# Performance work log

Measured on AMD Instinct MI355X. Metric: run time of the kernel, lower is better.

## Reference

```python
import jax, jax.numpy as jnp
import numpy as np

EPS = 1e-5

def conv1d(x, w, b, pad):
    # x: (B,Cin,T), w: (Cout,Cin,K)
    y = jax.lax.conv_general_dilated(x, w, (1,), [(pad, pad)],
                                     dimension_numbers=('NCW', 'OIW', 'NCW'))
    return y + b[None, :, None]

def group_norm(x, scale, bias, groups):
    B, C, T = x.shape
    xg = x.reshape(B, groups, C // groups, T)
    mu = xg.mean(axis=(2, 3), keepdims=True)
    var = xg.var(axis=(2, 3), keepdims=True)
    xn = ((xg - mu) * jax.lax.rsqrt(var + EPS)).reshape(B, C, T)
    return xn * scale[None, :, None] + bias[None, :, None]

def setup_inputs() -> dict:
    key = jax.random.key(0)
    ks = jax.random.split(key, 16)
    T, B = 1024, 128
    class_size, style_size, char_style_size = 80, 256, 64
    hidden, n_out = 128, 1
    cin = class_size + style_size + char_style_size  # 400
    def w(k, shape, fan_in):
        return jax.random.normal(k, shape, jnp.float32) * (1.0 / np.sqrt(fan_in))
    inp = {
        'input': jax.random.normal(ks[0], (T, B, class_size), jnp.float32),
        'g_style': jax.random.normal(ks[1], (B, style_size), jnp.float32),
        'spacing_style': jax.random.normal(ks[2], (B, 8), jnp.float32),
        'char_style': jax.random.normal(ks[3], (B, class_size, char_style_size), jnp.float32),
        'conv1_w': w(ks[4], (hidden, cin, 3), cin * 3),
        'conv1_b': jnp.zeros((hidden,), jnp.float32),
        'gn1_s': jnp.ones((hidden,), jnp.float32),
        'gn1_b': jnp.zeros((hidden,), jnp.float32),
        'conv2_w': w(ks[5], (hidden // 2, hidden, 3), hidden * 3),
        'conv2_b': jnp.zeros((hidden // 2,), jnp.float32),
        'gn2_s': jnp.ones((hidden // 2,), jnp.float32),
        'gn2_b': jnp.zeros((hidden // 2,), jnp.float32),
        'conv3_w': w(ks[6], (hidden // 4, hidden // 2, 3), (hidden // 2) * 3),
        'conv3_b': jnp.zeros((hidden // 4,), jnp.float32),
        'gn3_s': jnp.ones((hidden // 4,), jnp.float32),
        'gn3_b': jnp.zeros((hidden // 4,), jnp.float32),
        'conv4_w': w(ks[7], (n_out, hidden // 4, 1), hidden // 4),
        'conv4_b': jnp.zeros((n_out,), jnp.float32),
        'mean': jnp.full((1, n_out), 2.0, jnp.float32),
        'std': jnp.full((1, n_out), 1.0, jnp.float32),
    }
    return inp

def reference(input, g_style, spacing_style, char_style,
              conv1_w, conv1_b, gn1_s, gn1_b,
              conv2_w, conv2_b, gn2_s, gn2_b,
              conv3_w, conv3_b, gn3_s, gn3_b,
              conv4_w, conv4_b, mean, std):
    T, B, _ = input.shape
    # vectorized char-style gather (replaces the python double loop)
    text_chars = jnp.argmax(input, axis=2)                      # (T,B)
    input_style = char_style[jnp.arange(B)[None, :], text_chars]  # (T,B,Dc)
    gs = jnp.broadcast_to(g_style[None], (T,) + g_style.shape)    # (T,B,Ds)
    x = jnp.concatenate([input, gs, input_style], axis=2)         # (T,B,Cin)
    x = x.transpose(1, 2, 0)                                      # (B,Cin,T)
    x = jax.nn.relu(group_norm(conv1d(x, conv1_w, conv1_b, 1), gn1_s, gn1_b, 32))
    x = jax.nn.relu(group_norm(conv1d(x, conv2_w, conv2_b, 1), gn2_s, gn2_b, 32))
    x = jax.nn.relu(group_norm(conv1d(x, conv3_w, conv3_b, 1), gn3_s, gn3_b, 32))
    x = conv1d(x, conv4_w, conv4_b, 0)                            # (B,n_out,T)
    out = x.transpose(2, 0, 1)                                    # (T,B,n_out)
    return out * std + mean
```

## Files before the change

### kernel.cpp

```cpp
#include <hip/hip_runtime.h>
#include <hip/hip_bf16.h>

#define T_LEN 1024
#define BATCH 128
#define NM 131072

typedef __attribute__((ext_vector_type(8))) short short8;
typedef __attribute__((ext_vector_type(4))) float f32x4;

__device__ __forceinline__ float b2f(ushort u) {
  union { uint i; float f; } c; c.i = ((uint)u) << 16; return c.f;
}
__device__ __forceinline__ ushort f2b(float f) {
  __hip_bfloat16 h = __float2bfloat16(f);
  return *reinterpret_cast<ushort*>(&h);
}
__device__ __forceinline__ uint pack2(float a, float b) {
  return (uint)f2b(a) | ((uint)f2b(b) << 16);
}

__global__ __launch_bounds__(256) void k_prep(const float* __restrict__ inp, const float* __restrict__ cs,
    const float* __restrict__ gsty,
    const float* __restrict__ w1, const float* __restrict__ b1,
    const float* __restrict__ w2, const float* __restrict__ w3,
    ushort* __restrict__ X1, float* __restrict__ Gfull, float* __restrict__ Gk0, float* __restrict__ Gk2,
    ushort* __restrict__ Wp1, ushort* __restrict__ Wp2, ushort* __restrict__ Wp3) {
  int bid = blockIdx.x, tid = threadIdx.x;
  if (bid < 2048) {
    int m = bid * 64 + (tid >> 2);
    int q = tid & 3;
    int t = m >> 7, b = m & 127;
    const float* row = inp + (size_t)m * 80 + q * 20;
    float v[20];
    #pragma unroll
    for (int i = 0; i < 5; ++i) {
      float4 u = *(const float4*)(row + i*4);
      v[i*4+0]=u.x; v[i*4+1]=u.y; v[i*4+2]=u.z; v[i*4+3]=u.w;
    }
    float best = v[0]; int bi = q*20;
    #pragma unroll
    for (int i = 1; i < 20; ++i) if (v[i] > best) { best = v[i]; bi = q*20 + i; }
    #pragma unroll
    for (int d = 1; d <= 2; d <<= 1) {
      float ob = __shfl_xor(best, d);
      int   oi = __shfl_xor(bi, d);
      if (ob > best || (ob == best && oi < bi)) { best = ob; bi = oi; }
    }
    ushort* orow = X1 + ((size_t)b*1024 + t)*160;
    #pragma unroll
    for (int i = 0; i < 5; ++i) {
      uint2 pk; pk.x = pack2(v[i*4], v[i*4+1]); pk.y = pack2(v[i*4+2], v[i*4+3]);
      *(uint2*)(orow + q*20 + i*4) = pk;
    }
    *(uint2*)(orow + 80 + q*4) = make_uint2(0u, 0u);
    const float* crow = cs + ((size_t)b*80 + bi)*64 + q*16;
    #pragma unroll
    for (int i = 0; i < 4; ++i) {
      float4 u = *(const float4*)(crow + i*4);
      uint2 pk; pk.x = pack2(u.x, u.y); pk.y = pack2(u.z, u.w);
      *(uint2*)(orow + 96 + q*16 + i*4) = pk;
    }
  } else if (bid < 2176) {
    int b = bid - 2048;
    __shared__ float gl[256];
    gl[tid] = gsty[b*256 + tid];
    __syncthreads();
    if (tid < 128) {
      int o = tid;
      const float* wr = w1 + (size_t)o*1200 + 240;
      float s0 = 0.f, s1 = 0.f, s2 = 0.f;
      for (int c = 0; c < 256; ++c) {
        float g = gl[c];
        s0 += wr[c*3+0]*g; s1 += wr[c*3+1]*g; s2 += wr[c*3+2]*g;
      }
      Gk0[b*128+o] = s0;
      Gk2[b*128+o] = s2;
      Gfull[b*128+o] = s0 + s1 + s2 + b1[o];
    }
  } else {
    int e = (bid - 2176)*256 + tid;
    if (e < 61440) {
      int o = e / 480, r = e % 480, k = r / 160, c = r % 160;
      float v = 0.f;
      if (c < 80)       v = w1[(size_t)o*1200 + c*3 + k];
      else if (c >= 96) v = w1[(size_t)o*1200 + (336 + (c-96))*3 + k];
      Wp1[e] = f2b(v);
    } else if (e < 61440 + 24576) {
      int e2 = e - 61440;
      int o = e2/384, r = e2%384, k = r/128, c = r%128;
      Wp2[e2] = f2b(w2[(size_t)o*384 + c*3 + k]);
    } else if (e < 61440 + 24576 + 6144) {
      int e3 = e - 61440 - 24576;
      int o = e3/192, r = e3%192, k = r/64, c = r%64;
      Wp3[e3] = f2b(w3[(size_t)o*192 + c*3 + k]);
    }
  }
}

__device__ __forceinline__ uint4 c1_ldx(const ushort* X1b, int cc, int t0, int task) {
  int r = task >> 2, q = task & 3;
  int t = t0 - 1 + r;
  if (t >= 0 && t < T_LEN) return *(const uint4*)(X1b + (size_t)t*160 + cc*32 + q*8);
  return make_uint4(0u,0u,0u,0u);
}
__device__ __forceinline__ short8 c1_ldw(const ushort* Wp1, int cc, int task) {
  int o = task / 12, seg = task % 12;
  int k = seg >> 2, oct = seg & 3;
  return *(const short8*)(Wp1 + (size_t)o*480 + k*160 + cc*32 + oct*8);
}
__device__ __forceinline__ void c1_wrx(ushort (*Xsb)[40], int task, uint4 v) {
  int r = task >> 2, q = task & 3;
  *(uint4*)&Xsb[r][q*8] = v;
}
__device__ __forceinline__ void c1_wrw(ushort (*Wsb)[104], int task, short8 v) {
  int o = task / 12, seg = task % 12;
  *(short8*)&Wsb[o][seg*8] = v;
}

__global__ __launch_bounds__(256) void k_conv1(const ushort* __restrict__ X1, const ushort* __restrict__ Wp1,
    const float* __restrict__ Gfull, const float* __restrict__ Gk0, const float* __restrict__ Gk2,
    ushort* __restrict__ y1, float2* __restrict__ part1) {
  __shared__ __align__(16) ushort Xs[2][130][40];
  __shared__ __align__(16) ushort Ws[2][128][104];
  __shared__ float gf[128], g0v[128], g2v[128];
  __shared__ float ps[4][128], pq[4][128];
  int b = blockIdx.x, tt = blockIdx.y;
  int t0 = tt * 128;
  int tid = threadIdx.x, lane = tid & 63, wave = tid >> 6;
  int ln = lane & 15, lq = lane >> 4, wt = wave * 32;
  const ushort* X1b = X1 + (size_t)b * 163840;

  if (tid < 128) {
    gf[tid]  = Gfull[b*128 + tid];
    g0v[tid] = Gk0[b*128 + tid];
    g2v[tid] = Gk2[b*128 + tid];
  }
  f32x4 acc[2][8];
  #pragma unroll
  for (int m = 0; m < 2; ++m)
    #pragma unroll
    for (int n = 0; n < 8; ++n) { f32x4 z = {0.f,0.f,0.f,0.f}; acc[m][n] = z; }

  uint4 rx0, rx1, rx2;
  short8 rw[6];

  rx0 = c1_ldx(X1b, 0, t0, tid);
  rx1 = c1_ldx(X1b, 0, t0, tid + 256);
  if (tid < 8) rx2 = c1_ldx(X1b, 0, t0, tid + 512);
  #pragma unroll
  for (int i = 0; i < 6; ++i) rw[i] = c1_ldw(Wp1, 0, tid + i*256);
  c1_wrx(Xs[0], tid, rx0);
  c1_wrx(Xs[0], tid + 256, rx1);
  if (tid < 8) c1_wrx(Xs[0], tid + 512, rx2);
  #pragma unroll
  for (int i = 0; i < 6; ++i) c1_wrw(Ws[0], tid + i*256, rw[i]);
  __syncthreads();

  for (int cc = 0; cc < 5; ++cc) {
    bool more = (cc < 4);
    if (more) {
      rx0 = c1_ldx(X1b, cc+1, t0, tid);
      rx1 = c1_ldx(X1b, cc+1, t0, tid + 256);
      if (tid < 8) rx2 = c1_ldx(X1b, cc+1, t0, tid + 512);
      #pragma unroll
      for (int i = 0; i < 6; ++i) rw[i] = c1_ldw(Wp1, cc+1, tid + i*256);
    }
    int cur = cc & 1;
    #pragma unroll
    for (int k = 0; k < 3; ++k) {
      short8 a0 = *(const short8*)&Xs[cur][wt + ln + k][lq*8];
      short8 a1 = *(const short8*)&Xs[cur][wt + 16 + ln + k][lq*8];
      #pragma unroll
      for (int nt = 0; nt < 8; ++nt) {
        short8 bb = *(const short8*)&Ws[cur][nt*16 + ln][k*32 + lq*8];
        acc[0][nt] = __builtin_amdgcn_mfma_f32_16x16x32_bf16(a0, bb, acc[0][nt], 0, 0, 0);
        acc[1][nt] = __builtin_amdgcn_mfma_f32_16x16x32_bf16(a1, bb, acc[1][nt], 0, 0, 0);
      }
    }
    if (more) {
      int nxt = cur ^ 1;
      c1_wrx(Xs[nxt], tid, rx0);
      c1_wrx(Xs[nxt], tid + 256, rx1);
      if (tid < 8) c1_wrx(Xs[nxt], tid + 512, rx2);
      #pragma unroll
      for (int i = 0; i < 6; ++i) c1_wrw(Ws[nxt], tid + i*256, rw[i]);
    }
    __syncthreads();
  }

  #pragma unroll
  for (int nt = 0; nt < 8; ++nt) {
    int o = nt*16 + ln;
    float add = gf[o];
    float s = 0.f, sq = 0.f;
    #pragma unroll
    for (int mt = 0; mt < 2; ++mt) {
      int tb = t0 + wt + mt*16 + lq*4;
      float vv[4];
      #pragma unroll
      for (int r = 0; r < 4; ++r) {
        float v = acc[mt][nt][r] + add;
        int t = tb + r;
        if (t == 0) v -= g0v[o];
        if (t == T_LEN-1) v -= g2v[o];
        vv[r] = v; s += v; sq += v*v;
      }
      uint2 pk;
      pk.x = pack2(vv[0], vv[1]);
      pk.y = pack2(vv[2], vv[3]);
      *(uint2*)(y1 + ((size_t)b*128 + o)*T_LEN + tb) = pk;
    }
    s  += __shfl_xor(s, 16);  s  += __shfl_xor(s, 32);
    sq += __shfl_xor(sq, 16); sq += __shfl_xor(sq, 32);
    if (lane < 16) { ps[wave][o] = s; pq[wave][o] = sq; }
  }
  __syncthreads();
  if (tid < 128) {
    float S = ps[0][tid]+ps[1][tid]+ps[2][tid]+ps[3][tid];
    float Q = pq[0][tid]+pq[1][tid]+pq[2][tid]+pq[3][tid];
    part1[((size_t)b*128 + tid)*8 + tt] = make_float2(S, Q);
  }
}

__device__ __forceinline__ short8 mid_ldw(const ushort* Wp, int cin, int cc, int task) {
  int o = task / 12, seg = task % 12;
  int k = seg >> 2, oct = seg & 3;
  return *(const short8*)(Wp + ((size_t)o*3 + k)*cin + cc*32 + oct*8);
}
__device__ __forceinline__ void mid_wrw(ushort (*Wsb)[104], int task, short8 v) {
  int o = task / 12, seg = task % 12;
  *(short8*)&Wsb[o][seg*8] = v;
}

template<int NC, int CO, int NT, int CPG>
__global__ __launch_bounds__(256) void k_convmid(const ushort* __restrict__ xin,
    const ushort* __restrict__ Wp, const float* __restrict__ bias,
    const float2* __restrict__ partin, const float* __restrict__ gs, const float* __restrict__ gb,
    ushort* __restrict__ yout, float2* __restrict__ part) {
  constexpr int CIN = NC*32;
  constexpr int NG = CIN/CPG;
  __shared__ __align__(16) ushort Xs[2][130][40];
  __shared__ __align__(16) ushort Ws[2][CO][104];
  __shared__ float2 affl[CIN];
  __shared__ float ssb[CIN], qqb[CIN];
  __shared__ float2 gmr[NG];
  __shared__ float bl[CO];
  __shared__ float ps[4][CO], pq[4][CO];
  int b = blockIdx.x, tt = blockIdx.y, t0 = tt*128;
  int tid = threadIdx.x, lane = tid & 63, wave = tid >> 6;
  int ln = lane & 15, lq = lane >> 4, wt = wave*32;
  int cp = (tid & 15)*2, j = tid >> 4;
  int er = (tid < 32) ? 0 : 129, eci = tid & 31;
  const ushort* xb = xin + (size_t)b * CIN * T_LEN;

  if (tid < CIN) {
    const float2* p = partin + (size_t)(b*CIN + tid)*8;
    float S = 0.f, Q = 0.f;
    #pragma unroll
    for (int j2 = 0; j2 < 8; ++j2) { float2 v = p[j2]; S += v.x; Q += v.y; }
    ssb[tid] = S; qqb[tid] = Q;
  }
  if (tid < CO)  bl[tid]  = bias[tid];

  f32x4 acc[2][NT];
  #pragma unroll
  for (int m = 0; m < 2; ++m)
    #pragma unroll
    for (int n = 0; n < NT; ++n) { f32x4 z = {0.f,0.f,0.f,0.f}; acc[m][n] = z; }

  short8 v0, v1;
  ushort ev = 0;
  short8 rw0, rw1, rw2;
  int te = t0 - 1 + er;

  {
    const ushort* s0 = xb + (size_t)cp * T_LEN + t0 + j*8;
    v0 = *(const short8*)s0;
    v1 = *(const short8*)(s0 + T_LEN);
    ev = 0;
    if (tid < 64 && te >= 0 && te < T_LEN) ev = xb[(size_t)eci * T_LEN + te];
    rw0 = mid_ldw(Wp, CIN, 0, tid);
    if constexpr (CO == 64) {
      rw1 = mid_ldw(Wp, CIN, 0, tid + 256);
      rw2 = mid_ldw(Wp, CIN, 0, tid + 512);
    } else {
      if (tid < 128) rw1 = mid_ldw(Wp, CIN, 0, tid + 256);
    }
  }
  __syncthreads();
  if (tid < NG) {
    float S = 0.f, Q = 0.f;
    #pragma unroll
    for (int ci = 0; ci < CPG; ++ci) { S += ssb[tid*CPG+ci]; Q += qqb[tid*CPG+ci]; }
    float invn = 1.f / (float)(CPG * T_LEN);
    float m = S * invn;
    float var = Q * invn - m*m;
    gmr[tid] = make_float2(m, rsqrtf(var + 1e-5f));
  }
  __syncthreads();
  if (tid < CIN) {
    float2 mr = gmr[tid / CPG];
    float a = mr.y * gs[tid];
    affl[tid] = make_float2(a, gb[tid] - mr.x * a);
  }
  __syncthreads();
  {
    float2 A0 = affl[cp], A1 = affl[cp+1];
    #pragma unroll
    for (int e = 0; e < 8; ++e) {
      float f0 = fmaxf(0.f, b2f((ushort)v0[e])*A0.x + A0.y);
      float f1 = fmaxf(0.f, b2f((ushort)v1[e])*A1.x + A1.y);
      *(uint*)&Xs[0][1 + j*8 + e][cp] = pack2(f0, f1);
    }
    if (tid < 64) {
      ushort val = 0;
      if (te >= 0 && te < T_LEN) { float2 A = affl[eci]; val = f2b(fmaxf(0.f, b2f(ev)*A.x + A.y)); }
      Xs[0][er][eci] = val;
    }
    mid_wrw(Ws[0], tid, rw0);
    if constexpr (CO == 64) {
      mid_wrw(Ws[0], tid + 256, rw1);
      mid_wrw(Ws[0], tid + 512, rw2);
    } else {
      if (tid < 128) mid_wrw(Ws[0], tid + 256, rw1);
    }
  }
  __syncthreads();

  for (int cc = 0; cc < NC; ++cc) {
    bool more = (cc + 1 < NC);
    if (more) {
      const ushort* s0 = xb + (size_t)((cc+1)*32 + cp) * T_LEN + t0 + j*8;
      v0 = *(const short8*)s0;
      v1 = *(const short8*)(s0 + T_LEN);
      ev = 0;
      if (tid < 64 && te >= 0 && te < T_LEN) ev = xb[(size_t)((cc+1)*32 + eci) * T_LEN + te];
      rw0 = mid_ldw(Wp, CIN, cc+1, tid);
      if constexpr (CO == 64) {
        rw1 = mid_ldw(Wp, CIN, cc+1, tid + 256);
        rw2 = mid_ldw(Wp, CIN, cc+1, tid + 512);
      } else {
        if (tid < 128) rw1 = mid_ldw(Wp, CIN, cc+1, tid + 256);
      }
    }
    int cur = cc & 1;
    #pragma unroll
    for (int k = 0; k < 3; ++k) {
      short8 a0 = *(const short8*)&Xs[cur][wt + ln + k][lq*8];
      short8 a1 = *(const short8*)&Xs[cur][wt + 16 + ln + k][lq*8];
      #pragma unroll
      for (int nt = 0; nt < NT; ++nt) {
        short8 bb = *(const short8*)&Ws[cur][nt*16 + ln][k*32 + lq*8];
        acc[0][nt] = __builtin_amdgcn_mfma_f32_16x16x32_bf16(a0, bb, acc[0][nt], 0, 0, 0);
        acc[1][nt] = __builtin_amdgcn_mfma_f32_16x16x32_bf16(a1, bb, acc[1][nt], 0, 0, 0);
      }
    }
    if (more) {
      int nxt = cur ^ 1;
      float2 A0 = affl[(cc+1)*32 + cp], A1 = affl[(cc+1)*32 + cp + 1];
      #pragma unroll
      for (int e = 0; e < 8; ++e) {
        float f0 = fmaxf(0.f, b2f((ushort)v0[e])*A0.x + A0.y);
        float f1 = fmaxf(0.f, b2f((ushort)v1[e])*A1.x + A1.y);
        *(uint*)&Xs[nxt][1 + j*8 + e][cp] = pack2(f0, f1);
      }
      if (tid < 64) {
        ushort val = 0;
        if (te >= 0 && te < T_LEN) { float2 A = affl[(cc+1)*32 + eci]; val = f2b(fmaxf(0.f, b2f(ev)*A.x + A.y)); }
        Xs[nxt][er][eci] = val;
      }
      mid_wrw(Ws[nxt], tid, rw0);
      if constexpr (CO == 64) {
        mid_wrw(Ws[nxt], tid + 256, rw1);
        mid_wrw(Ws[nxt], tid + 512, rw2);
      } else {
        if (tid < 128) mid_wrw(Ws[nxt], tid + 256, rw1);
      }
    }
    __syncthreads();
  }

  #pragma unroll
  for (int nt = 0; nt < NT; ++nt) {
    int o = nt*16 + ln;
    float add = bl[o];
    float s = 0.f, sq = 0.f;
    #pragma unroll
    for (int mt = 0; mt < 2; ++mt) {
      int tb = t0 + wt + mt*16 + lq*4;
      float vv[4];
      #pragma unroll
      for (int r = 0; r < 4; ++r) {
        float v = acc[mt][nt][r] + add;
        vv[r] = v; s += v; sq += v*v;
      }
      uint2 pk;
      pk.x = pack2(vv[0], vv[1]);
      pk.y = pack2(vv[2], vv[3]);
      *(uint2*)(yout + ((size_t)b*CO + o)*T_LEN + tb) = pk;
    }
    s  += __shfl_xor(s, 16);  s  += __shfl_xor(s, 32);
    sq += __shfl_xor(sq, 16); sq += __shfl_xor(sq, 32);
    if (lane < 16) { ps[wave][o] = s; pq[wave][o] = sq; }
  }
  __syncthreads();
  if (tid < CO) {
    float S = ps[0][tid]+ps[1][tid]+ps[2][tid]+ps[3][tid];
    float Q = pq[0][tid]+pq[1][tid]+pq[2][tid]+pq[3][tid];
    part[((size_t)b*CO + tid)*8 + tt] = make_float2(S, Q);
  }
}

__global__ __launch_bounds__(256) void k_final(const ushort* __restrict__ y3, const float2* __restrict__ part3,
    const float* __restrict__ s3, const float* __restrict__ b3,
    const float* __restrict__ w4, const float* __restrict__ b4,
    const float* __restrict__ mn, const float* __restrict__ sd, float* __restrict__ out) {
  int b = blockIdx.x;
  int t = blockIdx.y * 256 + threadIdx.x;
  __shared__ float wl[32];
  __shared__ float2 al[32];
  if (threadIdx.x < 32) {
    int c = threadIdx.x;
    const float2* p = part3 + (size_t)(b*32 + c)*8;
    float S = 0.f, Q = 0.f;
    #pragma unroll
    for (int j = 0; j < 8; ++j) { float2 v = p[j]; S += v.x; Q += v.y; }
    float invn = 1.f / (float)T_LEN;
    float m = S * invn;
    float var = Q * invn - m*m;
    float rs = rsqrtf(var + 1e-5f);
    float a = rs * s3[c];
    al[c] = make_float2(a, b3[c] - m*a);
    wl[c] = w4[c];
  }
  __syncthreads();
  float s = b4[0];
  #pragma unroll 8
  for (int c = 0; c < 32; ++c) {
    float v = b2f(y3[((size_t)b*32 + c)*T_LEN + t]);
    float2 A = al[c];
    s += wl[c] * fmaxf(0.f, v*A.x + A.y);
  }
  out[(size_t)t*BATCH + b] = s*sd[0] + mn[0];
}

extern "C" void kernel_launch(void* const* d_in, const int* in_sizes, int n_in,
                              void* d_out, int out_size, void* d_ws, size_t ws_size,
                              hipStream_t stream) {
  const float* inp  = (const float*)d_in[0];
  const float* gsty = (const float*)d_in[1];
  const float* cs   = (const float*)d_in[3];
  const float* w1   = (const float*)d_in[4];
  const float* b1   = (const float*)d_in[5];
  const float* gn1s = (const float*)d_in[6];
  const float* gn1b = (const float*)d_in[7];
  const float* w2   = (const float*)d_in[8];
  const float* b2   = (const float*)d_in[9];
  const float* gn2s = (const float*)d_in[10];
  const float* gn2b = (const float*)d_in[11];
  const float* w3   = (const float*)d_in[12];
  const float* b3   = (const float*)d_in[13];
  const float* gn3s = (const float*)d_in[14];
  const float* gn3b = (const float*)d_in[15];
  const float* w4   = (const float*)d_in[16];
  const float* b4   = (const float*)d_in[17];
  const float* mn   = (const float*)d_in[18];
  const float* sd   = (const float*)d_in[19];
  float* out = (float*)d_out;
  ushort* wsu = (ushort*)d_ws;

  ushort* X1  = wsu;
  ushort* Wp1 = X1 + (size_t)20971520;
  ushort* Wp2 = Wp1 + 61440;
  ushort* Wp3 = Wp2 + 24576;
  float* Gfull = (float*)(Wp3 + 6144);
  float* Gk0   = Gfull + 16384;
  float* Gk2   = Gk0 + 16384;
  ushort* y1 = (ushort*)(Gk2 + 16384);
  ushort* y2 = y1 + (size_t)NM*128;
  ushort* y3 = y2 + (size_t)NM*64;
  float2* part1 = (float2*)(y3 + (size_t)NM*32);
  float2* part2 = part1 + 131072;
  float2* part3 = part2 + 65536;

  k_prep<<<2536, 256, 0, stream>>>(inp, cs, gsty, w1, b1, w2, w3,
                                   X1, Gfull, Gk0, Gk2, Wp1, Wp2, Wp3);
  k_conv1<<<dim3(128,8), 256, 0, stream>>>(X1, Wp1, Gfull, Gk0, Gk2, y1, part1);
  k_convmid<4,64,4,4><<<dim3(128,8), 256, 0, stream>>>(y1, Wp2, b2, part1, gn1s, gn1b, y2, part2);
  k_convmid<2,32,2,2><<<dim3(128,8), 256, 0, stream>>>(y2, Wp3, b3, part2, gn2s, gn2b, y3, part3);
  k_final<<<dim3(128,4), 256, 0, stream>>>(y3, part3, gn3s, gn3b, w4, b4, mn, sd, out);
}
```

Before: 98.53 us.

## Fuse input argmax/gather/concat staging into conv1 shared-memory load

Moves the argmax, char-style gather and bf16 packing of the conv1 input out of the prep kernel and into k_conv1, which now stages all 160 channels for its time tile (plus halo) directly into shared memory. This removes the write and re-read of the ~40MB X1 intermediate in global memory and shrinks the prep grid. In exchange, halo rows are recomputed by neighbouring tiles, the X tile is no longer double-buffered, and each conv1 block does more scattered fp32 loads up front before compute.

```diff
diff --git a/kernel.cpp b/kernel.cpp
--- a/kernel.cpp
+++ b/kernel.cpp
@@ -19,49 +19,14 @@
   return (uint)f2b(a) | ((uint)f2b(b) << 16);
 }
 
-__global__ __launch_bounds__(256) void k_prep(const float* __restrict__ inp, const float* __restrict__ cs,
-    const float* __restrict__ gsty,
+__global__ __launch_bounds__(256) void k_prep(const float* __restrict__ gsty,
     const float* __restrict__ w1, const float* __restrict__ b1,
     const float* __restrict__ w2, const float* __restrict__ w3,
-    ushort* __restrict__ X1, float* __restrict__ Gfull, float* __restrict__ Gk0, float* __restrict__ Gk2,
+    float* __restrict__ Gfull, float* __restrict__ Gk0, float* __restrict__ Gk2,
     ushort* __restrict__ Wp1, ushort* __restrict__ Wp2, ushort* __restrict__ Wp3) {
   int bid = blockIdx.x, tid = threadIdx.x;
-  if (bid < 2048) {
-    int m = bid * 64 + (tid >> 2);
-    int q = tid & 3;
-    int t = m >> 7, b = m & 127;
-    const float* row = inp + (size_t)m * 80 + q * 20;
-    float v[20];
-    #pragma unroll
-    for (int i = 0; i < 5; ++i) {
-      float4 u = *(const float4*)(row + i*4);
-      v[i*4+0]=u.x; v[i*4+1]=u.y; v[i*4+2]=u.z; v[i*4+3]=u.w;
-    }
-    float best = v[0]; int bi = q*20;
-    #pragma unroll
-    for (int i = 1; i < 20; ++i) if (v[i] > best) { best = v[i]; bi = q*20 + i; }
-    #pragma unroll
-    for (int d = 1; d <= 2; d <<= 1) {
-      float ob = __shfl_xor(best, d);
-      int   oi = __shfl_xor(bi, d);
-      if (ob > best || (ob == best && oi < bi)) { best = ob; bi = oi; }
-    }
-    ushort* orow = X1 + ((size_t)b*1024 + t)*160;
-    #pragma unroll
-    for (int i = 0; i < 5; ++i) {
-      uint2 pk; pk.x = pack2(v[i*4], v[i*4+1]); pk.y = pack2(v[i*4+2], v[i*4+3]);
-      *(uint2*)(orow + q*20 + i*4) = pk;
-    }
-    *(uint2*)(orow + 80 + q*4) = make_uint2(0u, 0u);
-    const float* crow = cs + ((size_t)b*80 + bi)*64 + q*16;
-    #pragma unroll
-    for (int i = 0; i < 4; ++i) {
-      float4 u = *(const float4*)(crow + i*4);
-      uint2 pk; pk.x = pack2(u.x, u.y); pk.y = pack2(u.z, u.w);
-      *(uint2*)(orow + 96 + q*16 + i*4) = pk;
-    }
-  } else if (bid < 2176) {
-    int b = bid - 2048;
+  if (bid < 128) {
+    int b = bid;
     __shared__ float gl[256];
     gl[tid] = gsty[b*256 + tid];
     __syncthreads();
@@ -78,7 +43,7 @@
       Gfull[b*128+o] = s0 + s1 + s2 + b1[o];
     }
   } else {
-    int e = (bid - 2176)*256 + tid;
+    int e = (bid - 128)*256 + tid;
     if (e < 61440) {
       int o = e / 480, r = e % 480, k = r / 160, c = r % 160;
       float v = 0.f;
@@ -97,30 +62,62 @@
   }
 }
 
-__device__ __forceinline__ uint4 c1_ldx(const ushort* X1b, int cc, int t0, int task) {
-  int r = task >> 2, q = task & 3;
-  int t = t0 - 1 + r;
-  if (t >= 0 && t < T_LEN) return *(const uint4*)(X1b + (size_t)t*160 + cc*32 + q*8);
-  return make_uint4(0u,0u,0u,0u);
-}
 __device__ __forceinline__ short8 c1_ldw(const ushort* Wp1, int cc, int task) {
   int o = task / 12, seg = task % 12;
   int k = seg >> 2, oct = seg & 3;
   return *(const short8*)(Wp1 + (size_t)o*480 + k*160 + cc*32 + oct*8);
 }
-__device__ __forceinline__ void c1_wrx(ushort (*Xsb)[40], int task, uint4 v) {
-  int r = task >> 2, q = task & 3;
-  *(uint4*)&Xsb[r][q*8] = v;
-}
 __device__ __forceinline__ void c1_wrw(ushort (*Wsb)[104], int task, short8 v) {
   int o = task / 12, seg = task % 12;
   *(short8*)&Wsb[o][seg*8] = v;
 }
 
-__global__ __launch_bounds__(256) void k_conv1(const ushort* __restrict__ X1, const ushort* __restrict__ Wp1,
+__device__ __forceinline__ void c1_stage_row(ushort* Xrow, const float* __restrict__ inp,
+                                             const float* __restrict__ cs, int b, int t, int q) {
+  if (t >= 0 && t < T_LEN) {
+    const float* rp = inp + ((size_t)t*128 + b)*80 + q*20;
+    float v[20];
+    #pragma unroll
+    for (int i = 0; i < 5; ++i) {
+      float4 u4 = *(const float4*)(rp + i*4);
+      v[i*4+0]=u4.x; v[i*4+1]=u4.y; v[i*4+2]=u4.z; v[i*4+3]=u4.w;
+    }
+    float best = v[0]; int bi = q*20;
+    #pragma unroll
+    for (int i = 1; i < 20; ++i) if (v[i] > best) { best = v[i]; bi = q*20 + i; }
+    #pragma unroll
+    for (int d = 1; d <= 2; d <<= 1) {
+      float ob = __shfl_xor(best, d);
+      int   oi = __shfl_xor(bi, d);
+      if (ob > best || (ob == best && oi < bi)) { best = ob; bi = oi; }
+    }
+    #pragma unroll
+    for (int i = 0; i < 5; ++i) {
+      uint2 pk; pk.x = pack2(v[i*4], v[i*4+1]); pk.y = pack2(v[i*4+2], v[i*4+3]);
+      *(uint2*)(Xrow + q*20 + i*4) = pk;
+    }
+    *(uint2*)(Xrow + 80 + q*4) = make_uint2(0u, 0u);
+    const float* crow = cs + ((size_t)b*80 + bi)*64 + q*16;
+    #pragma unroll
+    for (int i = 0; i < 4; ++i) {
+      float4 u4 = *(const float4*)(crow + i*4);
+      uint2 pk; pk.x = pack2(u4.x, u4.y); pk.y = pack2(u4.z, u4.w);
+      *(uint2*)(Xrow + 96 + q*16 + i*4) = pk;
+    }
+  } else {
+    #pragma unroll
+    for (int i = 0; i < 5; ++i) *(uint2*)(Xrow + q*20 + i*4) = make_uint2(0u, 0u);
+    *(uint2*)(Xrow + 80 + q*4) = make_uint2(0u, 0u);
+    #pragma unroll
+    for (int i = 0; i < 4; ++i) *(uint2*)(Xrow + 96 + q*16 + i*4) = make_uint2(0u, 0u);
+  }
+}
+
+__global__ __launch_bounds__(256) void k_conv1(const float* __restrict__ inp, const float* __restrict__ cs,
+    const ushort* __restrict__ Wp1,
     const float* __restrict__ Gfull, const float* __restrict__ Gk0, const float* __restrict__ Gk2,
     ushort* __restrict__ y1, float2* __restrict__ part1) {
-  __shared__ __align__(16) ushort Xs[2][130][40];
+  __shared__ __align__(16) ushort Xs[130][168];
   __shared__ __align__(16) ushort Ws[2][128][104];
   __shared__ float gf[128], g0v[128], g2v[128];
   __shared__ float ps[4][128], pq[4][128];
@@ -128,48 +125,45 @@
   int t0 = tt * 128;
   int tid = threadIdx.x, lane = tid & 63, wave = tid >> 6;
   int ln = lane & 15, lq = lane >> 4, wt = wave * 32;
-  const ushort* X1b = X1 + (size_t)b * 163840;
+  int q = tid & 3, u = tid >> 2;
+
+  short8 rw[6];
+  #pragma unroll
+  for (int i = 0; i < 6; ++i) rw[i] = c1_ldw(Wp1, 0, tid + i*256);
+
+  c1_stage_row(&Xs[u][0],      inp, cs, b, t0 - 1 + u,       q);
+  c1_stage_row(&Xs[u + 64][0], inp, cs, b, t0 - 1 + u + 64,  q);
+  if (tid < 8) {
+    int r = 128 + (tid >> 2);
+    c1_stage_row(&Xs[r][0], inp, cs, b, t0 - 1 + r, q);
+  }
 
   if (tid < 128) {
     gf[tid]  = Gfull[b*128 + tid];
     g0v[tid] = Gk0[b*128 + tid];
     g2v[tid] = Gk2[b*128 + tid];
   }
+  #pragma unroll
+  for (int i = 0; i < 6; ++i) c1_wrw(Ws[0], tid + i*256, rw[i]);
+
   f32x4 acc[2][8];
   #pragma unroll
   for (int m = 0; m < 2; ++m)
     #pragma unroll
     for (int n = 0; n < 8; ++n) { f32x4 z = {0.f,0.f,0.f,0.f}; acc[m][n] = z; }
-
-  uint4 rx0, rx1, rx2;
-  short8 rw[6];
-
-  rx0 = c1_ldx(X1b, 0, t0, tid);
-  rx1 = c1_ldx(X1b, 0, t0, tid + 256);
-  if (tid < 8) rx2 = c1_ldx(X1b, 0, t0, tid + 512);
-  #pragma unroll
-  for (int i = 0; i < 6; ++i) rw[i] = c1_ldw(Wp1, 0, tid + i*256);
-  c1_wrx(Xs[0], tid, rx0);
-  c1_wrx(Xs[0], tid + 256, rx1);
-  if (tid < 8) c1_wrx(Xs[0], tid + 512, rx2);
-  #pragma unroll
-  for (int i = 0; i < 6; ++i) c1_wrw(Ws[0], tid + i*256, rw[i]);
   __syncthreads();
 
   for (int cc = 0; cc < 5; ++cc) {
     bool more = (cc < 4);
     if (more) {
-      rx0 = c1_ldx(X1b, cc+1, t0, tid);
-      rx1 = c1_ldx(X1b, cc+1, t0, tid + 256);
-      if (tid < 8) rx2 = c1_ldx(X1b, cc+1, t0, tid + 512);
       #pragma unroll
       for (int i = 0; i < 6; ++i) rw[i] = c1_ldw(Wp1, cc+1, tid + i*256);
     }
     int cur = cc & 1;
     #pragma unroll
     for (int k = 0; k < 3; ++k) {
-      short8 a0 = *(const short8*)&Xs[cur][wt + ln + k][lq*8];
-      short8 a1 = *(const short8*)&Xs[cur][wt + 16 + ln + k][lq*8];
+      short8 a0 = *(const short8*)&Xs[wt + ln + k][cc*32 + lq*8];
+      short8 a1 = *(const short8*)&Xs[wt + 16 + ln + k][cc*32 + lq*8];
       #pragma unroll
       for (int nt = 0; nt < 8; ++nt) {
         short8 bb = *(const short8*)&Ws[cur][nt*16 + ln][k*32 + lq*8];
@@ -179,9 +173,6 @@
     }
     if (more) {
       int nxt = cur ^ 1;
-      c1_wrx(Xs[nxt], tid, rx0);
-      c1_wrx(Xs[nxt], tid + 256, rx1);
-      if (tid < 8) c1_wrx(Xs[nxt], tid + 512, rx2);
       #pragma unroll
       for (int i = 0; i < 6; ++i) c1_wrw(Ws[nxt], tid + i*256, rw[i]);
     }
@@ -469,8 +460,7 @@
   float* out = (float*)d_out;
   ushort* wsu = (ushort*)d_ws;
 
-  ushort* X1  = wsu;
-  ushort* Wp1 = X1 + (size_t)20971520;
+  ushort* Wp1 = wsu;
   ushort* Wp2 = Wp1 + 61440;
   ushort* Wp3 = Wp2 + 24576;
   float* Gfull = (float*)(Wp3 + 6144);
@@ -483,9 +473,9 @@
   float2* part2 = part1 + 131072;
   float2* part3 = part2 + 65536;
 
-  k_prep<<<2536, 256, 0, stream>>>(inp, cs, gsty, w1, b1, w2, w3,
-                                   X1, Gfull, Gk0, Gk2, Wp1, Wp2, Wp3);
-  k_conv1<<<dim3(128,8), 256, 0, stream>>>(X1, Wp1, Gfull, Gk0, Gk2, y1, part1);
+  k_prep<<<488, 256, 0, stream>>>(gsty, w1, b1, w2, w3,
+                                  Gfull, Gk0, Gk2, Wp1, Wp2, Wp3);
+  k_conv1<<<dim3(128,8), 256, 0, stream>>>(inp, cs, Wp1, Gfull, Gk0, Gk2, y1, part1);
   k_convmid<4,64,4,4><<<dim3(128,8), 256, 0, stream>>>(y1, Wp2, b2, part1, gn1s, gn1b, y2, part2);
   k_convmid<2,32,2,2><<<dim3(128,8), 256, 0, stream>>>(y2, Wp3, b3, part2, gn2s, gn2b, y3, part3);
   k_final<<<dim3(128,4), 256, 0, stream>>>(y3, part3, gn3s, gn3b, w4, b4, mn, sd, out);
```

After: 103.9 us. 1.05x slower.
